# Kernel optimization log

Measured on AMD Instinct MI355X. Metric: run time of the kernel, lower is better.

Reference implementation:

```python
import jax, jax.numpy as jnp
import numpy as np

NEG_SLOPE = 0.2  # PyG GATConv default


def setup_inputs() -> dict:
    key = jax.random.key(0)
    k1, k2, k3, k4, k5, k6 = jax.random.split(key, 6)
    N, F_in, F_out, E = 50000, 512, 256, 400000
    x = jax.random.normal(k1, (N, F_in), dtype=jnp.float32)
    adj = jax.random.randint(k2, (2, E), 0, N, dtype=jnp.int64)  # [2, E] edge_index (src, dst)
    glorot = lambda k, shape: jax.random.uniform(
        k, shape, jnp.float32, -1.0, 1.0) * np.sqrt(6.0 / (shape[0] + shape[-1]))
    W = glorot(k3, (F_in, F_out))
    att_src = glorot(k4, (F_out,))
    att_dst = glorot(k5, (F_out,))
    bias = jnp.zeros((F_out,), dtype=jnp.float32)
    return {"x": x, "adj": adj, "W": W, "att_src": att_src, "att_dst": att_dst, "bias": bias}


def reference(x, adj, W, att_src, att_dst, bias):
    N = x.shape[0]
    # add self loops (PyG GATConv default add_self_loops=True)
    loops = jnp.arange(N, dtype=adj.dtype)
    src = jnp.concatenate([adj[0], loops])
    dst = jnp.concatenate([adj[1], loops])

    h = x @ W                          # [N, F_out] projected features
    a_src = h @ att_src                # [N] per-node source attention term
    a_dst = h @ att_dst                # [N]
    e = a_src[src] + a_dst[dst]        # [E+N] edge logits
    e = jnp.where(e > 0, e, NEG_SLOPE * e)  # leaky_relu

    # per-destination softmax over incoming edges (numerically stable)
    m = jax.ops.segment_max(e, dst, num_segments=N)
    ex = jnp.exp(e - m[dst])
    denom = jax.ops.segment_sum(ex, dst, num_segments=N)
    alpha = ex / denom[dst]            # [E+N]

    # weighted scatter-aggregate of source messages
    out = jax.ops.segment_sum(alpha[:, None] * h[src], dst, num_segments=N)
    out = out + bias
    return jax.nn.relu(out)
```

## Files before the change

### kernel.cpp

```cpp
#include <hip/hip_runtime.h>
#include <hip/hip_bf16.h>

typedef __attribute__((ext_vector_type(8))) short bf16x8;
typedef __attribute__((ext_vector_type(4))) float f32x4;
typedef unsigned short u16;

#define F_IN 512
#define F_OUT 256
#define NEG_SLOPE 0.2f
#define CAP 64

__device__ __forceinline__ float leaky(float e) { return e > 0.f ? e : NEG_SLOPE * e; }

__device__ __forceinline__ u16 f2bf(float x) {
    __hip_bfloat16 h = __float2bfloat16(x);
    return *reinterpret_cast<u16*>(&h);
}
__device__ __forceinline__ void bf2x2(unsigned p, float& a, float& b) {
    a = __uint_as_float(p << 16);
    b = __uint_as_float(p & 0xffff0000u);
}

__device__ __forceinline__ void dma16(const void* g, void* l) {
    __builtin_amdgcn_global_load_lds((const __attribute__((address_space(1))) void*)g,
                                     (__attribute__((address_space(3))) void*)l, 16, 0, 0);
}

__global__ void k_transpose(const float* __restrict__ W, u16* __restrict__ Wt,
                            int* __restrict__ cnt, int N) {
    int t = blockIdx.x * 256 + threadIdx.x;
    int k = t >> 8;
    int n = t & 255;
    Wt[n * F_IN + k] = f2bf(W[k * F_OUT + n]);
    if (t < N) cnt[t] = 0;
}

__global__ __launch_bounds__(256) void k_gemm(const float* __restrict__ X,
                                              const u16* __restrict__ Wt,
                                              const float* __restrict__ att_src,
                                              const float* __restrict__ att_dst,
                                              u16* __restrict__ Hb,
                                              float* __restrict__ aS, float* __restrict__ aD,
                                              int N) {
    __shared__ float sA[64 * 32];
    __shared__ u16 sB[256 * 32];
    const int tid = threadIdx.x;
    const int wave = tid >> 6, lane = tid & 63;
    const int tile_m = blockIdx.x * 64;
    const int lm = lane & 15, q = lane >> 4;

    const int a_row_in = lane >> 3;
    const int a_gc = (lane & 7) ^ a_row_in;
    const float* aG[2];
#pragma unroll
    for (int t = 0; t < 2; ++t) {
        int grow = tile_m + wave * 16 + t * 8 + a_row_in;
        if (grow >= N) grow = N - 1;
        aG[t] = &X[(size_t)grow * F_IN + a_gc * 4];
    }
    const int b_col_in = lane >> 2;
    const int b_gc = (lane & 3) ^ (b_col_in & 3);
    const u16* bG[4];
#pragma unroll
    for (int t = 0; t < 4; ++t) {
        int col = wave * 64 + t * 16 + b_col_in;
        bG[t] = &Wt[(size_t)col * F_IN + b_gc * 8];
    }

    f32x4 acc[4][4];
#pragma unroll
    for (int i = 0; i < 4; i++)
#pragma unroll
        for (int j = 0; j < 4; j++) acc[i][j] = (f32x4){0.f, 0.f, 0.f, 0.f};

    for (int kb = 0; kb < F_IN / 32; ++kb) {
#pragma unroll
        for (int t = 0; t < 2; ++t)
            dma16(aG[t] + kb * 32, &sA[(wave * 16 + t * 8) * 32]);
#pragma unroll
        for (int t = 0; t < 4; ++t)
            dma16(bG[t] + kb * 32, &sB[(wave * 64 + t * 16) * 32]);
        __syncthreads();

        bf16x8 af[4], bfr[4];
#pragma unroll
        for (int i = 0; i < 4; i++) {
            const int arow = i * 16 + lm;
            const int s7 = lm & 7;
            const float4 c0 = *(const float4*)&sA[arow * 32 + (((2 * q) ^ s7) << 2)];
            const float4 c1 = *(const float4*)&sA[arow * 32 + (((2 * q + 1) ^ s7) << 2)];
            u16 a8[8] = {f2bf(c0.x), f2bf(c0.y), f2bf(c0.z), f2bf(c0.w),
                         f2bf(c1.x), f2bf(c1.y), f2bf(c1.z), f2bf(c1.w)};
            af[i] = *(const bf16x8*)a8;
        }
#pragma unroll
        for (int j = 0; j < 4; j++) {
            const int col = wave * 64 + j * 16 + lm;
            bfr[j] = *(const bf16x8*)&sB[col * 32 + ((q ^ (lm & 3)) << 3)];
        }
#pragma unroll
        for (int i = 0; i < 4; i++)
#pragma unroll
            for (int j = 0; j < 4; j++)
                acc[i][j] = __builtin_amdgcn_mfma_f32_16x16x32_bf16(af[i], bfr[j], acc[i][j], 0, 0, 0);
        __syncthreads();
    }

    float vS[4], vD[4];
#pragma unroll
    for (int j = 0; j < 4; ++j) {
        int col = wave * 64 + j * 16 + lm;
        vS[j] = att_src[col];
        vD[j] = att_dst[col];
    }
    float* sD = (float*)sA;
#pragma unroll
    for (int i = 0; i < 4; i++) {
#pragma unroll
        for (int r = 0; r < 4; r++) {
            float pS = acc[i][0][r] * vS[0] + acc[i][1][r] * vS[1] +
                       acc[i][2][r] * vS[2] + acc[i][3][r] * vS[3];
            float pD = acc[i][0][r] * vD[0] + acc[i][1][r] * vD[1] +
                       acc[i][2][r] * vD[2] + acc[i][3][r] * vD[3];
#pragma unroll
            for (int off = 1; off < 16; off <<= 1) {
                pS += __shfl_xor(pS, off);
                pD += __shfl_xor(pD, off);
            }
            if (lm == 0) {
                int rl = i * 16 + q * 4 + r;
                sD[rl * 8 + wave * 2 + 0] = pS;
                sD[rl * 8 + wave * 2 + 1] = pD;
            }
        }
    }
    __syncthreads();
    if (tid < 64) {
        int row = tile_m + tid;
        if (row < N) {
            aS[row] = sD[tid * 8 + 0] + sD[tid * 8 + 2] + sD[tid * 8 + 4] + sD[tid * 8 + 6];
            aD[row] = sD[tid * 8 + 1] + sD[tid * 8 + 3] + sD[tid * 8 + 5] + sD[tid * 8 + 7];
        }
    }

#pragma unroll
    for (int i = 0; i < 4; i++)
#pragma unroll
        for (int j = 0; j < 4; j++) {
#pragma unroll
            for (int r = 0; r < 4; r++) {
                int row = tile_m + i * 16 + q * 4 + r;
                int col = wave * 64 + j * 16 + lm;
                if (row < N) Hb[(size_t)row * F_OUT + col] = f2bf(acc[i][j][r]);
            }
        }
}

__global__ void k_scatter(const int* __restrict__ srcs, const int* __restrict__ dsts,
                          int* __restrict__ cnt, int* __restrict__ slots, int E) {
    int e = blockIdx.x * 256 + threadIdx.x;
    if (e >= E) return;
    int s = srcs[e], d = dsts[e];
    int pos = atomicAdd(&cnt[d], 1);
    if (pos < CAP) slots[(size_t)d * CAP + pos] = s;
}

__global__ __launch_bounds__(256) void k_aggregate(const u16* __restrict__ Hb,
                                                   const float* __restrict__ aS,
                                                   const float* __restrict__ aD,
                                                   const int* __restrict__ cnt,
                                                   const int* __restrict__ slots,
                                                   const float* __restrict__ bias,
                                                   float* __restrict__ out, int N) {
    int wave = threadIdx.x >> 6, lane = threadIdx.x & 63;
    int i = blockIdx.x * 4 + wave;
    if (i >= N) return;
    const float aDi = aD[i];
    float sex = __expf(leaky(aS[i] + aDi));

    uint2 rv = *(const uint2*)&Hb[(size_t)i * F_OUT + lane * 4];
    float f0, f1, f2, f3;
    bf2x2(rv.x, f0, f1);
    bf2x2(rv.y, f2, f3);
    float4 acc = {sex * f0, sex * f1, sex * f2, sex * f3};
    float wsum = sex;

    int end = cnt[i];
    if (end > CAP) end = CAP;
    const int* sl = &slots[(size_t)i * CAP];
    int k = 0;
    for (; k + 8 <= end; k += 8) {
        int ss[8];
        uint2 gg[8];
        float ww[8];
#pragma unroll
        for (int u = 0; u < 8; ++u) ss[u] = sl[k + u];
#pragma unroll
        for (int u = 0; u < 8; ++u)
            gg[u] = *(const uint2*)&Hb[(size_t)ss[u] * F_OUT + lane * 4];
#pragma unroll
        for (int u = 0; u < 8; ++u) ww[u] = __expf(leaky(aS[ss[u]] + aDi));
#pragma unroll
        for (int u = 0; u < 8; ++u) {
            wsum += ww[u];
            bf2x2(gg[u].x, f0, f1);
            bf2x2(gg[u].y, f2, f3);
            acc.x += ww[u] * f0; acc.y += ww[u] * f1;
            acc.z += ww[u] * f2; acc.w += ww[u] * f3;
        }
    }
    if (k + 4 <= end) {
        int ss[4];
        uint2 gg[4];
        float ww[4];
#pragma unroll
        for (int u = 0; u < 4; ++u) ss[u] = sl[k + u];
#pragma unroll
        for (int u = 0; u < 4; ++u)
            gg[u] = *(const uint2*)&Hb[(size_t)ss[u] * F_OUT + lane * 4];
#pragma unroll
        for (int u = 0; u < 4; ++u) ww[u] = __expf(leaky(aS[ss[u]] + aDi));
#pragma unroll
        for (int u = 0; u < 4; ++u) {
            wsum += ww[u];
            bf2x2(gg[u].x, f0, f1);
            bf2x2(gg[u].y, f2, f3);
            acc.x += ww[u] * f0; acc.y += ww[u] * f1;
            acc.z += ww[u] * f2; acc.w += ww[u] * f3;
        }
        k += 4;
    }
    for (; k < end; ++k) {
        int s = sl[k];
        float w = __expf(leaky(aS[s] + aDi));
        uint2 r = *(const uint2*)&Hb[(size_t)s * F_OUT + lane * 4];
        wsum += w;
        bf2x2(r.x, f0, f1);
        bf2x2(r.y, f2, f3);
        acc.x += w * f0;
        acc.y += w * f1;
        acc.z += w * f2;
        acc.w += w * f3;
    }
    float inv = 1.f / wsum;
    const float4 bv = *(const float4*)&bias[lane * 4];
    float4 o;
    o.x = acc.x * inv + bv.x;
    o.y = acc.y * inv + bv.y;
    o.z = acc.z * inv + bv.z;
    o.w = acc.w * inv + bv.w;
    o.x = o.x > 0.f ? o.x : 0.f;
    o.y = o.y > 0.f ? o.y : 0.f;
    o.z = o.z > 0.f ? o.z : 0.f;
    o.w = o.w > 0.f ? o.w : 0.f;
    *(float4*)&out[(size_t)i * F_OUT + lane * 4] = o;
}

extern "C" void kernel_launch(void* const* d_in, const int* in_sizes, int n_in,
                              void* d_out, int out_size, void* d_ws, size_t ws_size,
                              hipStream_t stream) {
    const float* X = (const float*)d_in[0];
    const int* adj = (const int*)d_in[1];
    const float* W = (const float*)d_in[2];
    const float* att_src = (const float*)d_in[3];
    const float* att_dst = (const float*)d_in[4];
    const float* bias = (const float*)d_in[5];
    float* out = (float*)d_out;

    const int N = in_sizes[0] / F_IN;
    const int E = in_sizes[1] / 2;
    const int* srcs = adj;
    const int* dsts = adj + E;

    char* p = (char*)d_ws;
    auto take = [&](size_t b) -> char* {
        char* q = p;
        p += (b + 255) & ~(size_t)255;
        return q;
    };
    u16* Hb = (u16*)take((size_t)N * F_OUT * sizeof(u16));
    u16* Wt = (u16*)take((size_t)F_IN * F_OUT * sizeof(u16));
    float* aS = (float*)take((size_t)N * sizeof(float));
    float* aD = (float*)take((size_t)N * sizeof(float));
    int* cnt = (int*)take((size_t)N * sizeof(int));
    int* slots = (int*)take((size_t)N * CAP * sizeof(int));

    k_transpose<<<(F_IN * F_OUT) / 256, 256, 0, stream>>>(W, Wt, cnt, N);
    k_gemm<<<(N + 63) / 64, 256, 0, stream>>>(X, Wt, att_src, att_dst, Hb, aS, aD, N);
    k_scatter<<<(E + 255) / 256, 256, 0, stream>>>(srcs, dsts, cnt, slots, E);
    k_aggregate<<<(N + 3) / 4, 256, 0, stream>>>(Hb, aS, aD, cnt, slots, bias, out, N);
}
```

Baseline: 265.5 us.

## Split aggregate wave into half-waves over edges and vectorize edge scatter

The aggregate kernel now splits each destination's wave into two 32-lane halves. Each half handles alternate incoming edges (self-loop included as index zero) with 16-byte row loads and four gathers in flight per iteration, then the halves are combined via lane shuffles. The scatter kernel reads four edges per thread with int4 loads to cut thread count. This aims to raise memory-level parallelism in the gather-bound aggregation, at the cost of padded iterations with zero weight and extra shuffle/register pressure.

New measurement: 264.0 us (median of 2 runs). No clear change (-0.6%).

```diff
diff --git a/kernel.cpp b/kernel.cpp
--- a/kernel.cpp
+++ b/kernel.cpp
@@ -158,11 +158,25 @@
 
 __global__ void k_scatter(const int* __restrict__ srcs, const int* __restrict__ dsts,
                           int* __restrict__ cnt, int* __restrict__ slots, int E) {
-    int e = blockIdx.x * 256 + threadIdx.x;
-    if (e >= E) return;
-    int s = srcs[e], d = dsts[e];
-    int pos = atomicAdd(&cnt[d], 1);
-    if (pos < CAP) slots[(size_t)d * CAP + pos] = s;
+    int e0 = (blockIdx.x * 256 + threadIdx.x) * 4;
+    if (e0 >= E) return;
+    if (e0 + 3 < E) {
+        int4 s4 = *(const int4*)&srcs[e0];
+        int4 d4 = *(const int4*)&dsts[e0];
+        int ss[4] = {s4.x, s4.y, s4.z, s4.w};
+        int dd[4] = {d4.x, d4.y, d4.z, d4.w};
+#pragma unroll
+        for (int u = 0; u < 4; ++u) {
+            int pos = atomicAdd(&cnt[dd[u]], 1);
+            if (pos < CAP) slots[(size_t)dd[u] * CAP + pos] = ss[u];
+        }
+    } else {
+        for (int e = e0; e < E; ++e) {
+            int s = srcs[e], d = dsts[e];
+            int pos = atomicAdd(&cnt[d], 1);
+            if (pos < CAP) slots[(size_t)d * CAP + pos] = s;
+        }
+    }
 }
 
 __global__ __launch_bounds__(256) void k_aggregate(const u16* __restrict__ Hb,
@@ -175,85 +189,74 @@
     int wave = threadIdx.x >> 6, lane = threadIdx.x & 63;
     int i = blockIdx.x * 4 + wave;
     if (i >= N) return;
+    const int half = lane >> 5, hl = lane & 31;
+    const int* sl = &slots[(size_t)i * CAP];
     const float aDi = aD[i];
-    float sex = __expf(leaky(aS[i] + aDi));
-
-    uint2 rv = *(const uint2*)&Hb[(size_t)i * F_OUT + lane * 4];
-    float f0, f1, f2, f3;
-    bf2x2(rv.x, f0, f1);
-    bf2x2(rv.y, f2, f3);
-    float4 acc = {sex * f0, sex * f1, sex * f2, sex * f3};
-    float wsum = sex;
-
     int end = cnt[i];
     if (end > CAP) end = CAP;
-    const int* sl = &slots[(size_t)i * CAP];
-    int k = 0;
-    for (; k + 8 <= end; k += 8) {
-        int ss[8];
-        uint2 gg[8];
-        float ww[8];
-#pragma unroll
-        for (int u = 0; u < 8; ++u) ss[u] = sl[k + u];
-#pragma unroll
-        for (int u = 0; u < 8; ++u)
-            gg[u] = *(const uint2*)&Hb[(size_t)ss[u] * F_OUT + lane * 4];
-#pragma unroll
-        for (int u = 0; u < 8; ++u) ww[u] = __expf(leaky(aS[ss[u]] + aDi));
-#pragma unroll
-        for (int u = 0; u < 8; ++u) {
-            wsum += ww[u];
-            bf2x2(gg[u].x, f0, f1);
-            bf2x2(gg[u].y, f2, f3);
-            acc.x += ww[u] * f0; acc.y += ww[u] * f1;
-            acc.z += ww[u] * f2; acc.w += ww[u] * f3;
-        }
-    }
-    if (k + 4 <= end) {
-        int ss[4];
-        uint2 gg[4];
-        float ww[4];
-#pragma unroll
-        for (int u = 0; u < 4; ++u) ss[u] = sl[k + u];
+    const int total = end + 1;
+
+    float a0 = 0.f, a1 = 0.f, a2 = 0.f, a3 = 0.f;
+    float a4 = 0.f, a5 = 0.f, a6 = 0.f, a7 = 0.f;
+    float wsum = 0.f;
+
+    for (int t = half; t < total; t += 8) {
+        int sarr[4];
+        uint4 g[4];
+        float warr[4];
+#pragma unroll
+        for (int u = 0; u < 4; ++u) {
+            int tt = t + 2 * u;
+            int idx = tt - 1;
+            idx = idx < 0 ? 0 : (idx >= CAP ? CAP - 1 : idx);
+            int sv = sl[idx];
+            int s = (tt == 0) ? i : sv;
+            sarr[u] = (tt < total) ? s : i;
+        }
 #pragma unroll
         for (int u = 0; u < 4; ++u)
-            gg[u] = *(const uint2*)&Hb[(size_t)ss[u] * F_OUT + lane * 4];
-#pragma unroll
-        for (int u = 0; u < 4; ++u) ww[u] = __expf(leaky(aS[ss[u]] + aDi));
-#pragma unroll
-        for (int u = 0; u < 4; ++u) {
-            wsum += ww[u];
-            bf2x2(gg[u].x, f0, f1);
-            bf2x2(gg[u].y, f2, f3);
-            acc.x += ww[u] * f0; acc.y += ww[u] * f1;
-            acc.z += ww[u] * f2; acc.w += ww[u] * f3;
-        }
-        k += 4;
-    }
-    for (; k < end; ++k) {
-        int s = sl[k];
-        float w = __expf(leaky(aS[s] + aDi));
-        uint2 r = *(const uint2*)&Hb[(size_t)s * F_OUT + lane * 4];
-        wsum += w;
-        bf2x2(r.x, f0, f1);
-        bf2x2(r.y, f2, f3);
-        acc.x += w * f0;
-        acc.y += w * f1;
-        acc.z += w * f2;
-        acc.w += w * f3;
-    }
+            g[u] = *(const uint4*)&Hb[(size_t)sarr[u] * F_OUT + hl * 8];
+#pragma unroll
+        for (int u = 0; u < 4; ++u) {
+            int tt = t + 2 * u;
+            warr[u] = (tt < total) ? __expf(leaky(aS[sarr[u]] + aDi)) : 0.f;
+        }
+#pragma unroll
+        for (int u = 0; u < 4; ++u) {
+            float c0, c1, c2, c3, c4, c5, c6, c7;
+            bf2x2(g[u].x, c0, c1);
+            bf2x2(g[u].y, c2, c3);
+            bf2x2(g[u].z, c4, c5);
+            bf2x2(g[u].w, c6, c7);
+            float w = warr[u];
+            wsum += w;
+            a0 += w * c0; a1 += w * c1; a2 += w * c2; a3 += w * c3;
+            a4 += w * c4; a5 += w * c5; a6 += w * c6; a7 += w * c7;
+        }
+    }
+
+    wsum += __shfl_xor(wsum, 32);
+    a0 += __shfl_xor(a0, 32); a1 += __shfl_xor(a1, 32);
+    a2 += __shfl_xor(a2, 32); a3 += __shfl_xor(a3, 32);
+    a4 += __shfl_xor(a4, 32); a5 += __shfl_xor(a5, 32);
+    a6 += __shfl_xor(a6, 32); a7 += __shfl_xor(a7, 32);
+
     float inv = 1.f / wsum;
-    const float4 bv = *(const float4*)&bias[lane * 4];
+    int col = hl * 8 + half * 4;
+    const float4 bv = *(const float4*)&bias[col];
     float4 o;
-    o.x = acc.x * inv + bv.x;
-    o.y = acc.y * inv + bv.y;
-    o.z = acc.z * inv + bv.z;
-    o.w = acc.w * inv + bv.w;
+    if (half == 0) {
+        o.x = a0 * inv + bv.x; o.y = a1 * inv + bv.y;
+        o.z = a2 * inv + bv.z; o.w = a3 * inv + bv.w;
+    } else {
+        o.x = a4 * inv + bv.x; o.y = a5 * inv + bv.y;
+        o.z = a6 * inv + bv.z; o.w = a7 * inv + bv.w;
+    }
     o.x = o.x > 0.f ? o.x : 0.f;
     o.y = o.y > 0.f ? o.y : 0.f;
     o.z = o.z > 0.f ? o.z : 0.f;
     o.w = o.w > 0.f ? o.w : 0.f;
-    *(float4*)&out[(size_t)i * F_OUT + lane * 4] = o;
+    *(float4*)&out[(size_t)i * F_OUT + col] = o;
 }
 
 extern "C" void kernel_launch(void* const* d_in, const int* in_sizes, int n_in,
@@ -283,10 +286,10 @@
     float* aS = (float*)take((size_t)N * sizeof(float));
     float* aD = (float*)take((size_t)N * sizeof(float));
     int* cnt = (int*)take((size_t)N * sizeof(int));
-    int* slots = (int*)take((size_t)N * CAP * sizeof(int));
+    int* slots = (int*)take(((size_t)N * CAP + 256) * sizeof(int));
 
     k_transpose<<<(F_IN * F_OUT) / 256, 256, 0, stream>>>(W, Wt, cnt, N);
     k_gemm<<<(N + 63) / 64, 256, 0, stream>>>(X, Wt, att_src, att_dst, Hb, aS, aD, N);
-    k_scatter<<<(E + 255) / 256, 256, 0, stream>>>(srcs, dsts, cnt, slots, E);
+    k_scatter<<<((E + 3) / 4 + 255) / 256, 256, 0, stream>>>(srcs, dsts, cnt, slots, E);
     k_aggregate<<<(N + 3) / 4, 256, 0, stream>>>(Hb, aS, aD, cnt, slots, bias, out, N);
 }
```
